# Kernel optimization log

Measured on AMD Instinct MI355X. Metric: run time of the kernel, lower is better.

## Reference

```python
import jax, jax.numpy as jnp
import numpy as np
from jax import lax

GAMMA = 0.01   # SoftDTWLossPyTorch(gamma=0.01)
INF = 1e10     # large finite sentinel for out-of-band DP cells (safe exp underflow)
C1 = 0.01 ** 2 # piqa SSIM constants, value_range=1
C2 = 0.03 ** 2


def _gauss_kernel(size=11, sigma=1.5):
    g = np.exp(-0.5 * ((np.arange(size) - (size - 1) / 2.0) / sigma) ** 2)
    g = g / g.sum()
    return jnp.asarray(np.outer(g, g).astype(np.float32))


def _blur(x, k2d):
    # depthwise valid Gaussian filter; x: [P, C, H, W]
    P, C, H, W = x.shape
    y = lax.conv_general_dilated(x.reshape(P * C, 1, H, W), k2d[None, None], (1, 1), 'VALID')
    return y.reshape(P, C, y.shape[-2], y.shape[-1])


def _ssim_pairs(x, y):
    # x, y: [P, 3, H, W] in [0,1]; returns per-pair mean SSIM [P] (piqa SSIM, reduction='none')
    k2d = _gauss_kernel()
    mu_x = _blur(x, k2d)
    mu_y = _blur(y, k2d)
    sxx = _blur(x * x, k2d) - mu_x ** 2
    syy = _blur(y * y, k2d) - mu_y ** 2
    sxy = _blur(x * y, k2d) - mu_x * mu_y
    num = (2.0 * mu_x * mu_y + C1) * (2.0 * sxy + C2)
    den = (mu_x ** 2 + mu_y ** 2 + C1) * (sxx + syy + C2)
    return (num / den).mean(axis=(1, 2, 3))


def _soft_dtw(x, y, gamma=GAMMA):
    # squared-euclidean soft-DTW for every (b, s) pair, wavefront over anti-diagonals
    # x: [B, T], y: [S, T] -> [B, S]
    B, T = x.shape
    S = y.shape[0]
    D = (x[:, None, :, None] - y[None, :, None, :]) ** 2  # [B, S, T, T]
    ii = jnp.arange(T)
    kk = jnp.arange(2 * T - 1)
    jj = kk[:, None] - ii[None, :]              # column index of cell i on diag k
    valid = (jj >= 0) & (jj < T)                # [2T-1, T]
    Dd = jnp.moveaxis(D[:, :, ii[None, :], jnp.clip(jj, 0, T - 1)], 2, 0)  # [2T-1, B, S, T]
    i0 = ii == 0

    def softmin3(a, b, c):
        m = jnp.minimum(jnp.minimum(a, b), c)
        return m - gamma * jnp.log(
            jnp.exp(-(a - m) / gamma) + jnp.exp(-(b - m) / gamma) + jnp.exp(-(c - m) / gamma))

    def step(carry, xs):
        r2, r1 = carry                     # diagonals k-2, k-1, each [B, S, T]
        d, v, k = xs
        pad = jnp.full(r1.shape[:-1] + (1,), INF, r1.dtype)
        r1s = jnp.concatenate([pad, r1[..., :-1]], axis=-1)  # R[i-1, j]
        r2s = jnp.concatenate([pad, r2[..., :-1]], axis=-1)  # R[i-1, j-1]
        sm = softmin3(r2s, r1s, r1)        # r1 itself is R[i, j-1]
        sm = jnp.where((k == 0) & i0, 0.0, sm)  # base cell R[0,0] = D[0,0]
        r = jnp.where(v, d + sm, INF)
        return (r1, r), None

    init = (jnp.full((B, S, T), INF, jnp.float32), jnp.full((B, S, T), INF, jnp.float32))
    (_, rf), _ = lax.scan(step, init, (Dd, valid, kk))
    return rf[..., -1]  # R[T-1, T-1]


def _forward(input, samples, img, sample_img, output, labels):
    B = input.shape[0]
    S = samples.shape[0]
    # all (sample, batch-image) pairs for SSIM; ssim(sample_img[i], img[b])
    X = jnp.broadcast_to(sample_img[None], (B,) + sample_img.shape).reshape((B * S,) + sample_img.shape[1:])
    Y = jnp.broadcast_to(img[:, None], (B, S) + img.shape[1:]).reshape((B * S,) + img.shape[1:])
    ssim = _ssim_pairs(X, Y).reshape(B, S)
    m0 = (1.0 - ssim) * 10.0
    m1 = _soft_dtw(input, samples) / 500.0
    per_b = ((m0 + m1) / 2.0).mean(axis=1)   # metrics.mean(dim=2).mean(dim=1)
    metric_sum = per_b.sum()
    # torch BCELoss with log clamped at -100
    ln = jnp.clip(jnp.log(output), -100.0, None)
    ln1 = jnp.clip(jnp.log1p(-output), -100.0, None)
    bce = -jnp.mean(labels * ln + (1.0 - labels) * ln1)
    loss = bce + metric_sum / 10.0
    return loss, bce, metric_sum


def setup_inputs() -> dict:
    key = jax.random.key(0)
    k1, k2, k3, k4, k5, k6 = jax.random.split(key, 6)
    B, S, T, H, W = 32, 8, 256, 128, 128
    return {
        'input': jax.random.normal(k1, (B, T), dtype=jnp.float32),
        'samples': jax.random.normal(k2, (S, T), dtype=jnp.float32),
        'img': jax.random.uniform(k3, (B, 3, H, W), dtype=jnp.float32),
        'sample_img': jax.random.uniform(k4, (S, 3, H, W), dtype=jnp.float32),
        'output': jax.random.uniform(k5, (B, 1), dtype=jnp.float32) * 0.98 + 0.01,
        'labels': (jax.random.uniform(k6, (B, 1)) < 0.5).astype(jnp.float32),
    }


def reference(input, samples, img, sample_img, output, labels):
    return _forward(input, samples, img, sample_img, output, labels)
```

## Files before the change

### kernel.cpp

```cpp
#include <hip/hip_runtime.h>
#include <math.h>

#define IW 128
#define OW 118
#define OWP 120
#define NPIX (IW*IW)
#define MOW (OW*OW)
#define NS 8
#define NB 32
#define NIMG 40
#define TT 256
#define SC1 0.0001f
#define SC2 0.0009f
#define NBAND 4
#define BROWS 30

__device__ __forceinline__ unsigned bfp(float x) {
    unsigned u = __float_as_uint(x);
    return (u + 0x7fffu + ((u >> 16) & 1u)) >> 16;
}
__device__ __forceinline__ float bflo(unsigned w) { return __uint_as_float(w << 16); }
__device__ __forceinline__ float bfhi(unsigned w) { return __uint_as_float(w & 0xffff0000u); }

__device__ __forceinline__ void gauss_regs(float* g) {
    float s = 0.f;
#pragma unroll
    for (int i = 0; i < 11; ++i) { float t = (i - 5) * (1.0f / 1.5f); g[i] = expf(-0.5f * t * t); s += g[i]; }
    float inv = 1.f / s;
#pragma unroll
    for (int i = 0; i < 11; ++i) g[i] *= inv;
}

#define CELLH(x_, y_, a_, b_, c_, out_) { float d_ = (x_) - (y_); \
    out_ = fmaf(d_, d_, fminf(fminf((a_), (b_)), (c_))); }

__global__ __launch_bounds__(256) void k_mom(const float* __restrict__ img,
        const float* __restrict__ simg, unsigned* __restrict__ MOM) {
    __shared__ float sR[NIMG * IW + 8];
    __shared__ float sHv[NIMG * OWP];
    __shared__ float sHs[NIMG * OWP];
    int cb = blockIdx.x, im = blockIdx.y;
    int ch = cb >> 2, band = cb & 3;
    int r0 = band * BROWS;
    int nrows = (118 - r0 < BROWS) ? (118 - r0) : BROWS;
    int in_rows = nrows + 10;
    const float* src = (im < NS) ? (simg + (size_t)(im * 3 + ch) * NPIX)
                                 : (img  + (size_t)((im - NS) * 3 + ch) * NPIX);
    float g[11]; gauss_regs(g);
    int t = threadIdx.x;
    for (int i4 = t; i4 < in_rows * (IW / 4); i4 += 256) {
        int r = i4 >> 5, c4 = i4 & 31;
        ((float4*)sR)[(r << 5) + c4] = ((const float4*)(src + (size_t)(r0 + r) * IW))[c4];
    }
    __syncthreads();
    {
        int cg = t & 31, tr = t >> 5;
        for (int rb = 0; rb < in_rows; rb += 8) {
            int r = rb + tr;
            if (r < in_rows && cg < 30) {
                const float* p = sR + r * IW + cg * 4;
                float4 A = *(const float4*)p, B = *(const float4*)(p + 4), C = *(const float4*)(p + 8);
                float2 D = *(const float2*)(p + 12);
                float w[14] = {A.x,A.y,A.z,A.w,B.x,B.y,B.z,B.w,C.x,C.y,C.z,C.w,D.x,D.y};
                float a0=0,a1=0,a2=0,a3=0,q0=0,q1=0,q2=0,q3=0;
#pragma unroll
                for (int k = 0; k < 11; ++k) {
                    float gk = g[k];
                    a0=fmaf(gk,w[k],a0); a1=fmaf(gk,w[k+1],a1); a2=fmaf(gk,w[k+2],a2); a3=fmaf(gk,w[k+3],a3);
                    q0=fmaf(gk,w[k]*w[k],q0); q1=fmaf(gk,w[k+1]*w[k+1],q1);
                    q2=fmaf(gk,w[k+2]*w[k+2],q2); q3=fmaf(gk,w[k+3]*w[k+3],q3);
                }
                *(float4*)(sHv + r * OWP + cg * 4) = make_float4(a0,a1,a2,a3);
                *(float4*)(sHs + r * OWP + cg * 4) = make_float4(q0,q1,q2,q3);
            }
        }
    }
    __syncthreads();
    unsigned* out = MOM + (size_t)(im * 3 + ch) * MOW;
    int c = t & 127, rg = t >> 7;
    if (c < 118) {
        for (int r = rg * 3; r < nrows; r += 6) {
            float a0=0,a1=0,a2=0,q0=0,q1=0,q2=0;
#pragma unroll
            for (int j = 0; j < 13; ++j) {
                float hv = sHv[(r + j) * OWP + c];
                float hq = sHs[(r + j) * OWP + c];
                if (j <= 10)           { float gv = g[j];     a0 = fmaf(gv, hv, a0); q0 = fmaf(gv, hq, q0); }
                if (j >= 1 && j <= 11) { float gv = g[j - 1]; a1 = fmaf(gv, hv, a1); q1 = fmaf(gv, hq, q1); }
                if (j >= 2)            { float gv = g[j - 2]; a2 = fmaf(gv, hv, a2); q2 = fmaf(gv, hq, q2); }
            }
            out[(size_t)(r0 + r) * OW + c] = bfp(a0) | (bfp(q0 - a0 * a0) << 16);
            if (r + 1 < nrows)
                out[(size_t)(r0 + r + 1) * OW + c] = bfp(a1) | (bfp(q1 - a1 * a1) << 16);
            if (r + 2 < nrows)
                out[(size_t)(r0 + r + 2) * OW + c] = bfp(a2) | (bfp(q2 - a2 * a2) << 16);
        }
    }
}

__global__ __launch_bounds__(256) void k_pairdtw(const float* __restrict__ img,
        const float* __restrict__ simg, const unsigned* __restrict__ MOM,
        float* __restrict__ SP, const float* __restrict__ input,
        const float* __restrict__ samples, float* __restrict__ dtw) {
    __shared__ float SM[NIMG * IW + 8];
    int bid = blockIdx.x;
    int t = threadIdx.x;
    if (bid < 64) {
        const float FINF = 1e10f;
        int w = t >> 6, l = t & 63;
        int pair = bid * 4 + w;
        int b = pair >> 3, s = pair & 7;
        float* sY = SM + (w << 8);
        *(float4*)(sY + l * 4) = *(const float4*)(samples + s * TT + l * 4);
        float4 xv = *(const float4*)(input + b * TT + l * 4);
        float x0 = xv.x, x1 = xv.y, x2 = xv.z, x3 = xv.w;
        __syncthreads();
        float left0 = FINF, left1 = FINF, left2 = FINF, left3 = FINF;
        float bot0 = FINF, bot1 = FINF, bot1p = FINF;
        for (int m = 0; m < 191; ++m) {
            float t0  = __shfl_up(bot0, 1);
            float t1  = __shfl_up(bot1, 1);
            float tdl = __shfl_up(bot1p, 1);
            if (l == 0) { t0 = FINF; t1 = FINF; tdl = FINF; }
            int c = m - l;
            if (0 <= c && c < 128) {
                float2 yv = *(const float2*)(sY + 2 * c);
                float y0 = yv.x, y1 = yv.y;
                bot1p = bot1;
                float up0 = t0, up1 = t1, dg = tdl, v0, v1;
                CELLH(x0, y0, dg, up0, left0, v0);
                if ((l | c) == 0) { float d0 = x0 - y0; v0 = d0 * d0; }
                CELLH(x0, y1, up0, up1, v0, v1);
                dg = left0; left0 = v1; up0 = v0; up1 = v1;
                CELLH(x1, y0, dg, up0, left1, v0);
                CELLH(x1, y1, up0, up1, v0, v1);
                dg = left1; left1 = v1; up0 = v0; up1 = v1;
                CELLH(x2, y0, dg, up0, left2, v0);
                CELLH(x2, y1, up0, up1, v0, v1);
                dg = left2; left2 = v1; up0 = v0; up1 = v1;
                CELLH(x3, y0, dg, up0, left3, v0);
                CELLH(x3, y1, up0, up1, v0, v1);
                left3 = v1; up0 = v0; up1 = v1;
                bot0 = up0; bot1 = up1;
            }
        }
        if (l == 63) dtw[pair] = bot1;
        return;
    }
    int pid = bid - 64;
    int xcd = pid & 7;
    int idx = pid >> 3;
    int q = (idx >= 288) ? 3 : (idx >= 192) ? 2 : (idx >= 96) ? 1 : 0;
    int rem = idx - q * 96;
    int b = xcd * 4 + q;
    int s = rem & 7;
    int cb = rem >> 3;
    int ch = cb >> 2, band = cb & 3;
    int r0 = band * BROWS;
    int nrows = (118 - r0 < BROWS) ? (118 - r0) : BROWS;
    int in_rows = nrows + 10;
    float* sP = SM;
    const float* xs = simg + (size_t)(s * 3 + ch) * NPIX;
    const float* ys = img  + (size_t)(b * 3 + ch) * NPIX;
    float g[11]; gauss_regs(g);
    for (int i4 = t; i4 < in_rows * (IW / 4); i4 += 256) {
        int r = i4 >> 5, c4 = i4 & 31;
        float4 xv = ((const float4*)(xs + (size_t)(r0 + r) * IW))[c4];
        float4 yv = ((const float4*)(ys + (size_t)(r0 + r) * IW))[c4];
        ((float4*)sP)[(r << 5) + c4] = make_float4(xv.x*yv.x, xv.y*yv.y, xv.z*yv.z, xv.w*yv.w);
    }
    __syncthreads();
    {
        int cg = t & 31, tr = t >> 5;
        for (int rb = 0; rb < in_rows; rb += 8) {
            int r = rb + tr;
            if (r < in_rows && cg < 30) {
                float* p = sP + r * IW + cg * 4;
                float4 A = *(const float4*)p, B = *(const float4*)(p + 4), C = *(const float4*)(p + 8);
                float2 D = *(const float2*)(p + 12);
                float w[14] = {A.x,A.y,A.z,A.w,B.x,B.y,B.z,B.w,C.x,C.y,C.z,C.w,D.x,D.y};
                float o0=0,o1=0,o2=0,o3=0;
#pragma unroll
                for (int k = 0; k < 11; ++k) {
                    float gk = g[k];
                    o0=fmaf(gk,w[k],o0); o1=fmaf(gk,w[k+1],o1); o2=fmaf(gk,w[k+2],o2); o3=fmaf(gk,w[k+3],o3);
                }
                *(float4*)p = make_float4(o0,o1,o2,o3);
            }
        }
    }
    __syncthreads();
    const unsigned* Mx = MOM + (size_t)(s * 3 + ch) * MOW;
    const unsigned* My = MOM + (size_t)((NS + b) * 3 + ch) * MOW;
    float lsum = 0.f;
    int c = t & 127, rg = t >> 7;
    if (c < 118) {
        for (int r = rg * 3; r < nrows; r += 6) {
            float a0=0,a1=0,a2=0;
#pragma unroll
            for (int j = 0; j < 13; ++j) {
                float h = sP[(r + j) * IW + c];
                if (j <= 10)           a0 = fmaf(g[j],     h, a0);
                if (j >= 1 && j <= 11) a1 = fmaf(g[j - 1], h, a1);
                if (j >= 2)            a2 = fmaf(g[j - 2], h, a2);
            }
            float bxy[3] = {a0, a1, a2};
#pragma unroll
            for (int o = 0; o < 3; ++o) {
                if (r + o < nrows) {
                    size_t gidx = (size_t)(r0 + r + o) * OW + c;
                    unsigned wx = Mx[gidx], wy = My[gidx];
                    float ux = bflo(wx), sxx = bfhi(wx);
                    float uy = bflo(wy), syy = bfhi(wy);
                    float sxy = bxy[o] - ux * uy;
                    float num = (2.f * ux * uy + SC1) * (2.f * sxy + SC2);
                    float den = (ux * ux + uy * uy + SC1) * (sxx + syy + SC2);
                    lsum += num * __builtin_amdgcn_rcpf(den);
                }
            }
        }
    }
#pragma unroll
    for (int off = 32; off > 0; off >>= 1) lsum += __shfl_down(lsum, off);
    __syncthreads();
    if ((t & 63) == 0) sP[t >> 6] = lsum;
    __syncthreads();
    int pair = b * 8 + s;
    if (t == 0) SP[((pair * 3) + ch) * NBAND + band] = sP[0] + sP[1] + sP[2] + sP[3];
}

__global__ __launch_bounds__(256) void k_final(const float* __restrict__ SP,
        const float* __restrict__ DTW, const float* __restrict__ outp,
        const float* __restrict__ lab, float* __restrict__ out) {
    __shared__ float redm[4], redb[4];
    int t = threadIdx.x;
    float ssum = 0.f;
#pragma unroll
    for (int i = 0; i < 3 * NBAND; ++i) ssum += SP[t * 3 * NBAND + i];
    float ssim = ssum * (1.0f / 41772.0f);
    float m0 = (1.f - ssim) * 10.f;
    float m1 = DTW[t] * (1.f / 500.f);
    float m = (m0 + m1) * 0.5f;
    float bt = 0.f;
    if (t < 32) {
        float o = outp[t], l = lab[t];
        float ln  = fmaxf(logf(o), -100.f);
        float ln1 = fmaxf(log1pf(-o), -100.f);
        bt = l * ln + (1.f - l) * ln1;
    }
#pragma unroll
    for (int off = 32; off > 0; off >>= 1) { m += __shfl_down(m, off); bt += __shfl_down(bt, off); }
    if ((t & 63) == 0) { redm[t >> 6] = m; redb[t >> 6] = bt; }
    __syncthreads();
    if (t == 0) {
        float msum = redm[0] + redm[1] + redm[2] + redm[3];
        float bsum = redb[0] + redb[1] + redb[2] + redb[3];
        float metric_sum = msum * 0.125f;
        float bce = -bsum * (1.f / 32.f);
        out[0] = bce + metric_sum * 0.1f;
        out[1] = bce;
        out[2] = metric_sum;
    }
}

extern "C" void kernel_launch(void* const* d_in, const int* in_sizes, int n_in,
                              void* d_out, int out_size, void* d_ws, size_t ws_size,
                              hipStream_t stream) {
    const float* input   = (const float*)d_in[0];
    const float* samples = (const float*)d_in[1];
    const float* img     = (const float*)d_in[2];
    const float* simg    = (const float*)d_in[3];
    const float* outp    = (const float*)d_in[4];
    const float* lab     = (const float*)d_in[5];
    float* out = (float*)d_out;
    unsigned* MOM = (unsigned*)d_ws;
    float* SP  = (float*)d_ws + (size_t)NIMG * 3 * MOW;
    float* DTW = SP + 256 * 3 * NBAND;

    k_mom    <<<dim3(12, 40),    dim3(256), 0, stream>>>(img, simg, MOM);
    k_pairdtw<<<dim3(64 + 3072), dim3(256), 0, stream>>>(img, simg, MOM, SP, input, samples, DTW);
    k_final  <<<dim3(1),         dim3(256), 0, stream>>>(SP, DTW, outp, lab, out);
}
```

Before: 116.1 us.

## Fuse moment blur into pair kernel with per-tile ready flags

Folds the per-image moment blur (mean and variance) into the combined SSIM/DTW kernel as extra blocks. These blocks publish per-tile release flags that the pair blocks spin on with acquire loads, so the pair blocks wait only for the tiles they need instead of for a whole kernel boundary. The moment blocks now reuse a single shared buffer and blur the squared image and the raw image one after the other, which lowers shared memory use at the cost of a second horizontal pass. The flags are never reset, so on later calls the pair blocks can read moment data from the previous call. Correctness also relies on producer blocks being scheduled before the consumers that spin on them.

```diff
diff --git a/kernel.cpp b/kernel.cpp
--- a/kernel.cpp
+++ b/kernel.cpp
@@ -3,7 +3,6 @@
 
 #define IW 128
 #define OW 118
-#define OWP 120
 #define NPIX (IW*IW)
 #define MOW (OW*OW)
 #define NS 8
@@ -14,6 +13,10 @@
 #define SC2 0.0009f
 #define NBAND 4
 #define BROWS 30
+#define NMOMBLK 480
+#define NSSIMBLK 3072
+#define GRIDSZ (64 + NMOMBLK + NSSIMBLK)
+#define FLAG_SET 1u
 
 __device__ __forceinline__ unsigned bfp(float x) {
     unsigned u = __float_as_uint(x);
@@ -34,74 +37,31 @@
 #define CELLH(x_, y_, a_, b_, c_, out_) { float d_ = (x_) - (y_); \
     out_ = fmaf(d_, d_, fminf(fminf((a_), (b_)), (c_))); }
 
-__global__ __launch_bounds__(256) void k_mom(const float* __restrict__ img,
-        const float* __restrict__ simg, unsigned* __restrict__ MOM) {
-    __shared__ float sR[NIMG * IW + 8];
-    __shared__ float sHv[NIMG * OWP];
-    __shared__ float sHs[NIMG * OWP];
-    int cb = blockIdx.x, im = blockIdx.y;
-    int ch = cb >> 2, band = cb & 3;
-    int r0 = band * BROWS;
-    int nrows = (118 - r0 < BROWS) ? (118 - r0) : BROWS;
-    int in_rows = nrows + 10;
-    const float* src = (im < NS) ? (simg + (size_t)(im * 3 + ch) * NPIX)
-                                 : (img  + (size_t)((im - NS) * 3 + ch) * NPIX);
-    float g[11]; gauss_regs(g);
-    int t = threadIdx.x;
-    for (int i4 = t; i4 < in_rows * (IW / 4); i4 += 256) {
-        int r = i4 >> 5, c4 = i4 & 31;
-        ((float4*)sR)[(r << 5) + c4] = ((const float4*)(src + (size_t)(r0 + r) * IW))[c4];
-    }
-    __syncthreads();
-    {
-        int cg = t & 31, tr = t >> 5;
-        for (int rb = 0; rb < in_rows; rb += 8) {
-            int r = rb + tr;
-            if (r < in_rows && cg < 30) {
-                const float* p = sR + r * IW + cg * 4;
-                float4 A = *(const float4*)p, B = *(const float4*)(p + 4), C = *(const float4*)(p + 8);
-                float2 D = *(const float2*)(p + 12);
-                float w[14] = {A.x,A.y,A.z,A.w,B.x,B.y,B.z,B.w,C.x,C.y,C.z,C.w,D.x,D.y};
-                float a0=0,a1=0,a2=0,a3=0,q0=0,q1=0,q2=0,q3=0;
-#pragma unroll
-                for (int k = 0; k < 11; ++k) {
-                    float gk = g[k];
-                    a0=fmaf(gk,w[k],a0); a1=fmaf(gk,w[k+1],a1); a2=fmaf(gk,w[k+2],a2); a3=fmaf(gk,w[k+3],a3);
-                    q0=fmaf(gk,w[k]*w[k],q0); q1=fmaf(gk,w[k+1]*w[k+1],q1);
-                    q2=fmaf(gk,w[k+2]*w[k+2],q2); q3=fmaf(gk,w[k+3]*w[k+3],q3);
-                }
-                *(float4*)(sHv + r * OWP + cg * 4) = make_float4(a0,a1,a2,a3);
-                *(float4*)(sHs + r * OWP + cg * 4) = make_float4(q0,q1,q2,q3);
-            }
-        }
-    }
-    __syncthreads();
-    unsigned* out = MOM + (size_t)(im * 3 + ch) * MOW;
-    int c = t & 127, rg = t >> 7;
-    if (c < 118) {
-        for (int r = rg * 3; r < nrows; r += 6) {
-            float a0=0,a1=0,a2=0,q0=0,q1=0,q2=0;
-#pragma unroll
-            for (int j = 0; j < 13; ++j) {
-                float hv = sHv[(r + j) * OWP + c];
-                float hq = sHs[(r + j) * OWP + c];
-                if (j <= 10)           { float gv = g[j];     a0 = fmaf(gv, hv, a0); q0 = fmaf(gv, hq, q0); }
-                if (j >= 1 && j <= 11) { float gv = g[j - 1]; a1 = fmaf(gv, hv, a1); q1 = fmaf(gv, hq, q1); }
-                if (j >= 2)            { float gv = g[j - 2]; a2 = fmaf(gv, hv, a2); q2 = fmaf(gv, hq, q2); }
-            }
-            out[(size_t)(r0 + r) * OW + c] = bfp(a0) | (bfp(q0 - a0 * a0) << 16);
-            if (r + 1 < nrows)
-                out[(size_t)(r0 + r + 1) * OW + c] = bfp(a1) | (bfp(q1 - a1 * a1) << 16);
-            if (r + 2 < nrows)
-                out[(size_t)(r0 + r + 2) * OW + c] = bfp(a2) | (bfp(q2 - a2 * a2) << 16);
-        }
-    }
-}
-
-__global__ __launch_bounds__(256) void k_pairdtw(const float* __restrict__ img,
-        const float* __restrict__ simg, const unsigned* __restrict__ MOM,
+__device__ __forceinline__ void hblur_inplace(float* sP, int in_rows, const float* g, int t) {
+    int cg = t & 31, tr = t >> 5;
+    for (int rb = 0; rb < in_rows; rb += 8) {
+        int r = rb + tr;
+        if (r < in_rows && cg < 30) {
+            float* p = sP + r * IW + cg * 4;
+            float4 A = *(const float4*)p, B = *(const float4*)(p + 4), C = *(const float4*)(p + 8);
+            float2 D = *(const float2*)(p + 12);
+            float w[14] = {A.x,A.y,A.z,A.w,B.x,B.y,B.z,B.w,C.x,C.y,C.z,C.w,D.x,D.y};
+            float o0=0,o1=0,o2=0,o3=0;
+#pragma unroll
+            for (int k = 0; k < 11; ++k) {
+                float gk = g[k];
+                o0=fmaf(gk,w[k],o0); o1=fmaf(gk,w[k+1],o1); o2=fmaf(gk,w[k+2],o2); o3=fmaf(gk,w[k+3],o3);
+            }
+            *(float4*)p = make_float4(o0,o1,o2,o3);
+        }
+    }
+}
+
+__global__ __launch_bounds__(256) void k_fused(const float* __restrict__ img,
+        const float* __restrict__ simg, unsigned* __restrict__ MOM,
         float* __restrict__ SP, const float* __restrict__ input,
-        const float* __restrict__ samples, float* __restrict__ dtw) {
+        const float* __restrict__ samples, float* __restrict__ dtw,
+        unsigned* __restrict__ flags) {
     __shared__ float SM[NIMG * IW + 8];
     int bid = blockIdx.x;
     int t = threadIdx.x;
@@ -147,7 +107,79 @@
         if (l == 63) dtw[pair] = bot1;
         return;
     }
-    int pid = bid - 64;
+    if (bid < 64 + NMOMBLK) {
+        int id = bid - 64;
+        int im = id % 40, cb = id / 40;
+        int ch = cb >> 2, band = cb & 3;
+        int r0 = band * BROWS;
+        int nrows = (118 - r0 < BROWS) ? (118 - r0) : BROWS;
+        int in_rows = nrows + 10;
+        const float* src = (im < NS) ? (simg + (size_t)(im * 3 + ch) * NPIX)
+                                     : (img  + (size_t)((im - NS) * 3 + ch) * NPIX);
+        float g[11]; gauss_regs(g);
+        float* sP = SM;
+        int c = t & 127, rg = t >> 7;
+        float qa[15];
+        for (int i4 = t; i4 < in_rows * (IW / 4); i4 += 256) {
+            int r = i4 >> 5, c4 = i4 & 31;
+            float4 v = ((const float4*)(src + (size_t)(r0 + r) * IW))[c4];
+            ((float4*)sP)[(r << 5) + c4] = make_float4(v.x*v.x, v.y*v.y, v.z*v.z, v.w*v.w);
+        }
+        __syncthreads();
+        hblur_inplace(sP, in_rows, g, t);
+        __syncthreads();
+        if (c < 118) {
+#pragma unroll
+            for (int it = 0; it < 5; ++it) {
+                int r = rg * 3 + it * 6;
+                float a0=0,a1=0,a2=0;
+#pragma unroll
+                for (int j = 0; j < 13; ++j) {
+                    float h = sP[(r + j) * IW + c];
+                    if (j <= 10)           a0 = fmaf(g[j],     h, a0);
+                    if (j >= 1 && j <= 11) a1 = fmaf(g[j - 1], h, a1);
+                    if (j >= 2)            a2 = fmaf(g[j - 2], h, a2);
+                }
+                qa[it*3+0]=a0; qa[it*3+1]=a1; qa[it*3+2]=a2;
+            }
+        }
+        __syncthreads();
+        for (int i4 = t; i4 < in_rows * (IW / 4); i4 += 256) {
+            int r = i4 >> 5, c4 = i4 & 31;
+            ((float4*)sP)[(r << 5) + c4] = ((const float4*)(src + (size_t)(r0 + r) * IW))[c4];
+        }
+        __syncthreads();
+        hblur_inplace(sP, in_rows, g, t);
+        __syncthreads();
+        unsigned* outm = MOM + (size_t)(im * 3 + ch) * MOW;
+        if (c < 118) {
+#pragma unroll
+            for (int it = 0; it < 5; ++it) {
+                int r = rg * 3 + it * 6;
+                float a0=0,a1=0,a2=0;
+#pragma unroll
+                for (int j = 0; j < 13; ++j) {
+                    float h = sP[(r + j) * IW + c];
+                    if (j <= 10)           a0 = fmaf(g[j],     h, a0);
+                    if (j >= 1 && j <= 11) a1 = fmaf(g[j - 1], h, a1);
+                    if (j >= 2)            a2 = fmaf(g[j - 2], h, a2);
+                }
+                float mm[3] = {a0, a1, a2};
+#pragma unroll
+                for (int o = 0; o < 3; ++o) {
+                    if (r + o < nrows) {
+                        float m = mm[o], var = qa[it*3+o] - m * m;
+                        outm[(size_t)(r0 + r + o) * OW + c] = bfp(m) | (bfp(var) << 16);
+                    }
+                }
+            }
+        }
+        __syncthreads();
+        if (t == 0)
+            __hip_atomic_store(&flags[id], FLAG_SET, __ATOMIC_RELEASE, __HIP_MEMORY_SCOPE_AGENT);
+        return;
+    }
+    int pid = bid - (64 + NMOMBLK);
     int xcd = pid & 7;
     int idx = pid >> 3;
     int q = (idx >= 288) ? 3 : (idx >= 192) ? 2 : (idx >= 96) ? 1 : 0;
@@ -170,24 +202,12 @@
         ((float4*)sP)[(r << 5) + c4] = make_float4(xv.x*yv.x, xv.y*yv.y, xv.z*yv.z, xv.w*yv.w);
     }
     __syncthreads();
-    {
-        int cg = t & 31, tr = t >> 5;
-        for (int rb = 0; rb < in_rows; rb += 8) {
-            int r = rb + tr;
-            if (r < in_rows && cg < 30) {
-                float* p = sP + r * IW + cg * 4;
-                float4 A = *(const float4*)p, B = *(const float4*)(p + 4), C = *(const float4*)(p + 8);
-                float2 D = *(const float2*)(p + 12);
-                float w[14] = {A.x,A.y,A.z,A.w,B.x,B.y,B.z,B.w,C.x,C.y,C.z,C.w,D.x,D.y};
-                float o0=0,o1=0,o2=0,o3=0;
-#pragma unroll
-                for (int k = 0; k < 11; ++k) {
-                    float gk = g[k];
-                    o0=fmaf(gk,w[k],o0); o1=fmaf(gk,w[k+1],o1); o2=fmaf(gk,w[k+2],o2); o3=fmaf(gk,w[k+3],o3);
-                }
-                *(float4*)p = make_float4(o0,o1,o2,o3);
-            }
-        }
+    hblur_inplace(sP, in_rows, g, t);
+    __syncthreads();
+    if (t < 2) {
+        int f = cb * 40 + ((t == 0) ? s : (8 + b));
+        while (__hip_atomic_load(&flags[f], __ATOMIC_ACQUIRE, __HIP_MEMORY_SCOPE_AGENT) != FLAG_SET)
+            __builtin_amdgcn_s_sleep(8);
     }
     __syncthreads();
     const unsigned* Mx = MOM + (size_t)(s * 3 + ch) * MOW;
@@ -276,8 +296,8 @@
     unsigned* MOM = (unsigned*)d_ws;
     float* SP  = (float*)d_ws + (size_t)NIMG * 3 * MOW;
     float* DTW = SP + 256 * 3 * NBAND;
-
-    k_mom    <<<dim3(12, 40),    dim3(256), 0, stream>>>(img, simg, MOM);
-    k_pairdtw<<<dim3(64 + 3072), dim3(256), 0, stream>>>(img, simg, MOM, SP, input, samples, DTW);
-    k_final  <<<dim3(1),         dim3(256), 0, stream>>>(SP, DTW, outp, lab, out);
-}
+    unsigned* FLAGS = (unsigned*)(DTW + 256);
+
+    k_fused<<<dim3(GRIDSZ), dim3(256), 0, stream>>>(img, simg, MOM, SP, input, samples, DTW, FLAGS);
+    k_final<<<dim3(1),      dim3(256), 0, stream>>>(SP, DTW, outp, lab, out);
+}
```

Result: slower. 153.2 us (+31.9%).
